# Optimization experiments

Measured on AMD Instinct MI355X. Metric: run time of the kernel, lower is better.

The kernel has to match this reference:

```python
import jax, jax.numpy as jnp
import numpy as np

N = 100_000
E = 1_600_000
IN_DIM = 21
HID = 256
OUT = 256


def setup_inputs() -> dict:
    key = jax.random.key(0)
    ks = jax.random.split(key, 10)
    node_scalar = jax.random.normal(ks[0], (N, IN_DIM), dtype=jnp.float32)
    edge_index = jax.random.randint(ks[1], (2, E), 0, N, dtype=jnp.int64)
    s_in = 1.0 / np.sqrt(IN_DIM)
    s_h = 1.0 / np.sqrt(HID)
    W_in = jax.random.uniform(ks[2], (IN_DIM, HID), jnp.float32, -s_in, s_in)
    b_in = jax.random.uniform(ks[3], (HID,), jnp.float32, -s_in, s_in)
    W_self = jax.random.uniform(ks[4], (HID, HID), jnp.float32, -s_h, s_h)
    b_self = jax.random.uniform(ks[5], (HID,), jnp.float32, -s_h, s_h)
    W_nei = jax.random.uniform(ks[6], (HID, HID), jnp.float32, -s_h, s_h)
    b_nei = jax.random.uniform(ks[7], (HID,), jnp.float32, -s_h, s_h)
    W_out = jax.random.uniform(ks[8], (HID, OUT), jnp.float32, -s_h, s_h)
    b_out = jax.random.uniform(ks[9], (OUT,), jnp.float32, -s_h, s_h)
    return {
        "node_scalar": node_scalar,
        "W_in": W_in, "b_in": b_in,
        "W_self": W_self, "b_self": b_self,
        "W_nei": W_nei, "b_nei": b_nei,
        "W_out": W_out, "b_out": b_out,
        "edge_index": edge_index,
    }


def reference(node_scalar, W_in, b_in, W_self, b_self, W_nei, b_nei, W_out, b_out, edge_index):
    # x = relu(Linear(node_scalar)); dropout is identity in eval mode
    x = jax.nn.relu(node_scalar @ W_in + b_in)           # (N, H)
    n = x.shape[0]
    src, dst = edge_index[0], edge_index[1]
    msg = x[src]                                          # (E, H) gather
    agg = jax.ops.segment_sum(msg, dst, num_segments=n)   # (N, H) scatter-add
    deg = jax.ops.segment_sum(jnp.ones((dst.shape[0],), dtype=x.dtype), dst, num_segments=n)
    agg = agg / jnp.maximum(deg, 1.0)[:, None]            # degree mean (clamp_min 1)
    h = jax.nn.relu(x @ W_self + b_self + agg @ W_nei + b_nei)
    g = h.mean(axis=0)                                    # global mean pool -> (H,)
    return g @ W_out + b_out                              # (OUT,)
```

## Files before the change

### kernel.cpp

```cpp
#include <hip/hip_runtime.h>
#include <hip/hip_bf16.h>

#define HID 256
#define IND 21
#define PB 6400
#define MAXB 512

typedef short short8 __attribute__((ext_vector_type(8)));
typedef float floatx16 __attribute__((ext_vector_type(16)));
typedef float floatx2 __attribute__((ext_vector_type(2)));

__device__ inline unsigned short f2bf(float f) {
  __hip_bfloat16 h = __float2bfloat16(f);
  union { __hip_bfloat16 h; unsigned short u; } c;
  c.h = h;
  return c.u;
}

__device__ inline unsigned int pk_bf16_trunc(floatx2 p) {
  union { float f; unsigned int u; } a, b;
  a.f = p.x; b.f = p.y;
  return (b.u & 0xffff0000u) | (a.u >> 16);
}

__device__ inline void acc8p(uint2 v, floatx2* a) {
  a[0] += __builtin_amdgcn_cvt_pk_f32_fp8((int)v.x, false);
  a[1] += __builtin_amdgcn_cvt_pk_f32_fp8((int)v.x, true);
  a[2] += __builtin_amdgcn_cvt_pk_f32_fp8((int)v.y, false);
  a[3] += __builtin_amdgcn_cvt_pk_f32_fp8((int)v.y, true);
}

__device__ inline short8 mk_s8(unsigned a, unsigned b, unsigned c, unsigned d) {
  union { uint4 u; short8 s; } x; x.u = make_uint4(a, b, c, d); return x.s;
}

__device__ inline short8 dec8(uint2 v) {
  unsigned w0 = pk_bf16_trunc(__builtin_amdgcn_cvt_pk_f32_fp8((int)v.x, false));
  unsigned w1 = pk_bf16_trunc(__builtin_amdgcn_cvt_pk_f32_fp8((int)v.x, true));
  unsigned w2 = pk_bf16_trunc(__builtin_amdgcn_cvt_pk_f32_fp8((int)v.y, false));
  unsigned w3 = pk_bf16_trunc(__builtin_amdgcn_cvt_pk_f32_fp8((int)v.y, true));
  return mk_s8(w0, w1, w2, w3);
}

__device__ inline void gl16(const unsigned char* g, unsigned char* l) {
  __builtin_amdgcn_global_load_lds(
      (const __attribute__((address_space(1))) unsigned char*)g,
      (__attribute__((address_space(3))) unsigned char*)l, 16, 0, 0);
}

__global__ __launch_bounds__(256) void k_front(
    const float* __restrict__ ns, const float* __restrict__ Win,
    const float* __restrict__ bin, uint2* __restrict__ xq2,
    uint2* __restrict__ Aqx,
    const float* __restrict__ Wself, const float* __restrict__ Wnei,
    unsigned short* __restrict__ Bf16,
    const int* __restrict__ dst, int* __restrict__ bcnt,
    int N, int E, int nb2, int G1) {
  int blk = blockIdx.x;
  int tid = threadIdx.x;
  if (blk < G1) {
    __shared__ float s[8][IND];
    __shared__ float fx[8][257];
    int nb = blk * 8;
    if (tid < 8 * IND) {
      int idx = nb * IND + tid;
      s[tid / IND][tid % IND] = (idx < N * IND) ? ns[idx] : 0.f;
    }
    float w[IND];
#pragma unroll
    for (int k = 0; k < IND; k++) w[k] = Win[k * HID + tid];
    float b = bin[tid];
    __syncthreads();
#pragma unroll
    for (int j = 0; j < 8; j++) {
      float acc = b;
#pragma unroll
      for (int k = 0; k < IND; k++) acc += s[j][k] * w[k];
      fx[j][tid] = acc > 0.f ? acc : 0.f;
    }
    __syncthreads();
    {
      int j = tid & 7, u = tid >> 3;
      int node = nb + j;
      if (node < N) {
        const float* fp = &fx[j][u * 8];
        int lo0 = __builtin_amdgcn_cvt_pk_fp8_f32(fp[0], fp[1], 0, false);
        int w0  = __builtin_amdgcn_cvt_pk_fp8_f32(fp[2], fp[3], lo0, true);
        int lo1 = __builtin_amdgcn_cvt_pk_fp8_f32(fp[4], fp[5], 0, false);
        int w1  = __builtin_amdgcn_cvt_pk_fp8_f32(fp[6], fp[7], lo1, true);
        uint2 val = make_uint2((unsigned)w0, (unsigned)w1);
        xq2[(size_t)node * 32 + u] = val;
        int g = node >> 5, row = node & 31, c = u >> 1, hi = u & 1;
        Aqx[(size_t)(g * 16 + c) * 64 + hi * 32 + row] = val;
      }
    }
  } else if (blk < G1 + 256) {
    int n = blk - G1;
    int ct = n >> 5, l5 = n & 31;
#pragma unroll
    for (int t = 0; t < 2; t++) {
      int k = tid + t * 256;
      float v = (k < HID) ? Wself[k * HID + n] : Wnei[(k - HID) * HID + n];
      int c = k >> 4, kin = k & 15;
      int lane = (kin >> 3) * 32 + l5;
      int j = kin & 7;
      Bf16[(size_t)((c * 8 + ct) * 64 + lane) * 8 + j] = f2bf(v);
    }
  } else {
    __shared__ int lh[MAXB];
    int e0 = (blk - G1 - 256) * PB;
    for (int b = tid; b < nb2; b += 256) lh[b] = 0;
    __syncthreads();
    int c = min(PB, E - e0);
    for (int i = tid; i < c; i += 256) atomicAdd(&lh[dst[e0 + i] >> 8], 1);
    __syncthreads();
    for (int b = tid; b < nb2; b += 256)
      if (lh[b]) atomicAdd(&bcnt[b], lh[b]);
  }
}

__global__ __launch_bounds__(512) void k_bscan(
    const int* __restrict__ bcnt, int* __restrict__ bbase, int* __restrict__ bcur,
    int* __restrict__ row_start, int E, int N, int nb2) {
  __shared__ int ts[512];
  int tid = threadIdx.x;
  int v = (tid < nb2) ? bcnt[tid] : 0;
  ts[tid] = v;
  __syncthreads();
  for (int off = 1; off < 512; off <<= 1) {
    int t = (tid >= off) ? ts[tid - off] : 0;
    __syncthreads();
    ts[tid] += t;
    __syncthreads();
  }
  if (tid < nb2) { bbase[tid] = ts[tid] - v; bcur[tid] = ts[tid] - v; }
  if (tid == 0) { bbase[nb2] = E; row_start[N] = E; }
}

__global__ __launch_bounds__(256) void k_part(
    const int* __restrict__ src, const int* __restrict__ dst,
    int* __restrict__ bcur, unsigned int* __restrict__ ebuf, int E, int nb2) {
  __shared__ int lh[MAXB];
  int tid = threadIdx.x;
  int e0 = blockIdx.x * PB;
  for (int b = tid; b < nb2; b += 256) lh[b] = 0;
  __syncthreads();
  int cnt = min(PB, E - e0);
  for (int i = tid; i < cnt; i += 256) atomicAdd(&lh[dst[e0 + i] >> 8], 1);
  __syncthreads();
  for (int b = tid; b < nb2; b += 256) {
    int c = lh[b];
    lh[b] = (c > 0) ? atomicAdd(&bcur[b], c) : 0;
  }
  __syncthreads();
  for (int i = tid; i < cnt; i += 256) {
    int s = src[e0 + i];
    int d = dst[e0 + i];
    int pos = atomicAdd(&lh[d >> 8], 1);
    ebuf[pos] = ((unsigned)s << 8) | ((unsigned)d & 255u);
  }
}

__global__ __launch_bounds__(256) void k_fill2(
    const unsigned int* __restrict__ ebuf, const int* __restrict__ bbase,
    int* __restrict__ row_start, unsigned int* __restrict__ csr, int N) {
  __shared__ int lcnt[256];
  __shared__ int lcur[256];
  __shared__ int ts[256];
  int b = blockIdx.x;
  int tid = threadIdx.x;
  int start = bbase[b], end = bbase[b + 1];
  lcnt[tid] = 0;
  __syncthreads();
  for (int i = start + tid; i < end; i += 256)
    atomicAdd(&lcnt[ebuf[i] & 255u], 1);
  __syncthreads();
  int v = lcnt[tid];
  ts[tid] = v;
  __syncthreads();
  for (int off = 1; off < 256; off <<= 1) {
    int t = (tid >= off) ? ts[tid - off] : 0;
    __syncthreads();
    ts[tid] += t;
    __syncthreads();
  }
  int excl = start + ts[tid] - v;
  int node = (b << 8) + tid;
  if (node < N) row_start[node] = excl;
  lcur[tid] = excl;
  __syncthreads();
  for (int i = start + tid; i < end; i += 256) {
    unsigned int e = ebuf[i];
    int pos = atomicAdd(&lcur[e & 255u], 1);
    csr[pos] = e & ~255u;
  }
}

__global__ __launch_bounds__(256) void k_agg(
    const unsigned char* __restrict__ xqb, const unsigned int* __restrict__ csrb,
    const int* __restrict__ row_start, uint2* __restrict__ Aqagg, int N) {
  __shared__ uint2 ld[8][33];
  int tid = threadIdx.x;
  int lane = tid & 63;
  int w = tid >> 6;
  int half = lane >> 5;
  int l32 = lane & 31;
  unsigned lo = (unsigned)(l32 * 8);

  int nl = w * 2 + half;
  int wid = blockIdx.x * 8 + nl;
  int cw = (wid < N) ? wid : (N - 1);
  int start = row_start[cw];
  int end = row_start[cw + 1];
  int c = end - start;
  floatx2 a[4], b[4], d[4], e[4];
#pragma unroll
  for (int j = 0; j < 4; j++) {
    a[j] = (floatx2){0.f, 0.f}; b[j] = (floatx2){0.f, 0.f};
    d[j] = (floatx2){0.f, 0.f}; e[j] = (floatx2){0.f, 0.f};
  }
  int i = 0;
  while (i < c) {
    int nb = min(32, c - i);
    int sel = (l32 < nb) ? l32 : 0;
    unsigned idx = csrb[start + i + sel];
    int j = 0;
    for (; j + 8 <= nb; j += 8) {
      unsigned o0 = (unsigned)__shfl((int)idx, j + 0, 32) + lo;
      unsigned o1 = (unsigned)__shfl((int)idx, j + 1, 32) + lo;
      unsigned o2 = (unsigned)__shfl((int)idx, j + 2, 32) + lo;
      unsigned o3 = (unsigned)__shfl((int)idx, j + 3, 32) + lo;
      unsigned o4 = (unsigned)__shfl((int)idx, j + 4, 32) + lo;
      unsigned o5 = (unsigned)__shfl((int)idx, j + 5, 32) + lo;
      unsigned o6 = (unsigned)__shfl((int)idx, j + 6, 32) + lo;
      unsigned o7 = (unsigned)__shfl((int)idx, j + 7, 32) + lo;
      uint2 v0 = *(const uint2*)(xqb + o0);
      uint2 v1 = *(const uint2*)(xqb + o1);
      uint2 v2 = *(const uint2*)(xqb + o2);
      uint2 v3 = *(const uint2*)(xqb + o3);
      uint2 v4 = *(const uint2*)(xqb + o4);
      uint2 v5 = *(const uint2*)(xqb + o5);
      uint2 v6 = *(const uint2*)(xqb + o6);
      uint2 v7 = *(const uint2*)(xqb + o7);
      acc8p(v0, a); acc8p(v1, b); acc8p(v2, d); acc8p(v3, e);
      acc8p(v4, a); acc8p(v5, b); acc8p(v6, d); acc8p(v7, e);
    }
    for (; j + 4 <= nb; j += 4) {
      unsigned o0 = (unsigned)__shfl((int)idx, j + 0, 32) + lo;
      unsigned o1 = (unsigned)__shfl((int)idx, j + 1, 32) + lo;
      unsigned o2 = (unsigned)__shfl((int)idx, j + 2, 32) + lo;
      unsigned o3 = (unsigned)__shfl((int)idx, j + 3, 32) + lo;
      uint2 v0 = *(const uint2*)(xqb + o0);
      uint2 v1 = *(const uint2*)(xqb + o1);
      uint2 v2 = *(const uint2*)(xqb + o2);
      uint2 v3 = *(const uint2*)(xqb + o3);
      acc8p(v0, a); acc8p(v1, b); acc8p(v2, d); acc8p(v3, e);
    }
    for (; j < nb; j++) {
      unsigned o0 = (unsigned)__shfl((int)idx, j, 32) + lo;
      uint2 v0 = *(const uint2*)(xqb + o0);
      acc8p(v0, a);
    }
    i += nb;
  }
#pragma unroll
  for (int j = 0; j < 4; j++) a[j] += b[j] + d[j] + e[j];

  float inv = 1.0f / fmaxf((float)c, 1.0f);
  float f[8];
#pragma unroll
  for (int j = 0; j < 4; j++) {
    f[2 * j] = a[j].x * inv;
    f[2 * j + 1] = a[j].y * inv;
  }
  int lo0 = __builtin_amdgcn_cvt_pk_fp8_f32(f[0], f[1], 0, false);
  int w0  = __builtin_amdgcn_cvt_pk_fp8_f32(f[2], f[3], lo0, true);
  int lo1 = __builtin_amdgcn_cvt_pk_fp8_f32(f[4], f[5], 0, false);
  int w1  = __builtin_amdgcn_cvt_pk_fp8_f32(f[6], f[7], lo1, true);
  ld[nl][l32] = make_uint2((unsigned)w0, (unsigned)w1);
  __syncthreads();

  int g = blockIdx.x >> 2;
  int r0 = (blockIdx.x & 3) * 8;
  int s = tid >> 3, j = tid & 7;
  Aqagg[(size_t)g * 1024 + (size_t)s * 32 + r0 + j] = ld[j][s];
}

__global__ __launch_bounds__(256, 3) void k_h(
    const unsigned char* __restrict__ Aqx, const unsigned char* __restrict__ Aqagg,
    const unsigned char* __restrict__ Bf8, const float* __restrict__ bself,
    const float* __restrict__ bnei, float* __restrict__ gsum, int N, int nfull) {
  __shared__ __align__(16) unsigned char As[2][8192];
  __shared__ __align__(16) unsigned char Bs[2][16384];
  __shared__ float colsum[128];
  int bid = blockIdx.x;
  int bx, by;
  if (bid < nfull) {
    bx = (bid >> 4) * 8 + (bid & 7);
    by = (bid >> 3) & 1;
  } else {
    int rem = bid - nfull;
    bx = (nfull >> 1) + (rem >> 1);
    by = rem & 1;
  }
  int tid = threadIdx.x;
  int lane = tid & 63;
  int w = tid >> 6;
  int wr = w >> 1, wc = w & 1;
  int l32 = lane & 31, half = lane >> 5;
  int rowBase = bx * 128;

  if (tid < 128) colsum[tid] = 0.f;

  floatx16 acc[2][2];
#pragma unroll
  for (int i = 0; i < 2; i++)
#pragma unroll
    for (int j = 0; j < 2; j++) acc[i][j] = (floatx16)(0.f);

  size_t a_grp = (size_t)(bx * 4 + w) * 16 * 512;
  int lb = lane * 16;

  {
    const unsigned char* asrc = Aqx + a_grp + lb;
    gl16(asrc, As[0] + w * 2048);
    gl16(asrc + 1024, As[0] + w * 2048 + 1024);
#pragma unroll
    for (int fi = 0; fi < 4; fi++) {
      int ctg = by * 4 + fi;
      gl16(Bf8 + (size_t)(w * 8 + ctg) * 1024 + lb, Bs[0] + (w * 4 + fi) * 1024);
    }
  }

  for (int ch = 0; ch < 8; ch++) {
    int buf = ch & 1;
    __syncthreads();
    if (ch < 7) {
      int cn = ch + 1;
      const unsigned char* Aq = (cn < 4) ? Aqx : Aqagg;
      const unsigned char* asrc = Aq + a_grp + (size_t)(cn & 3) * 2048 + lb;
      unsigned char* ad = As[buf ^ 1] + w * 2048;
      gl16(asrc, ad);
      gl16(asrc + 1024, ad + 1024);
#pragma unroll
      for (int fi = 0; fi < 4; fi++) {
        int cg = cn * 4 + w;
        int ctg = by * 4 + fi;
        gl16(Bf8 + (size_t)(cg * 8 + ctg) * 1024 + lb,
             Bs[buf ^ 1] + (w * 4 + fi) * 1024);
      }
    }
#pragma unroll
    for (int cl = 0; cl < 4; cl++) {
      short8 afr[2];
#pragma unroll
      for (int rt = 0; rt < 2; rt++) {
        uint2 av = *(const uint2*)&As[buf][(wr * 2 + rt) * 2048 + cl * 512 + lane * 8];
        afr[rt] = dec8(av);
      }
#pragma unroll
      for (int ctw = 0; ctw < 2; ctw++) {
        short8 bfr = *(const short8*)&Bs[buf][(cl * 4 + wc * 2 + ctw) * 1024 + lane * 16];
#pragma unroll
        for (int rt = 0; rt < 2; rt++)
          acc[rt][ctw] = __builtin_amdgcn_mfma_f32_32x32x16_bf16(
              afr[rt], bfr, acc[rt][ctw], 0, 0, 0);
      }
    }
  }

#pragma unroll
  for (int ctw = 0; ctw < 2; ctw++) {
    int lcol = (wc * 2 + ctw) * 32 + l32;
    int gcol = by * 128 + lcol;
    float bb = bself[gcol] + bnei[gcol];
    float psum = 0.f;
#pragma unroll
    for (int rt = 0; rt < 2; rt++) {
#pragma unroll
      for (int r = 0; r < 16; r++) {
        int rw = rowBase + wr * 64 + rt * 32 + (r & 3) + 8 * (r >> 2) + 4 * half;
        float v = acc[rt][ctw][r] + bb;
        v = v > 0.f ? v : 0.f;
        if (rw < N) psum += v;
      }
    }
    atomicAdd(&colsum[lcol], psum);
  }
  __syncthreads();
  if (tid < 128) atomicAdd(&gsum[by * 128 + tid], colsum[tid]);
}

__global__ __launch_bounds__(HID) void k_out(
    const float* __restrict__ gsum, const float* __restrict__ Wout,
    const float* __restrict__ bout, float* __restrict__ out, float invN) {
  __shared__ float g[HID];
  int c = threadIdx.x;
  g[c] = gsum[c] * invN;
  __syncthreads();
  float acc = bout[c];
#pragma unroll 8
  for (int k = 0; k < HID; k++) acc += g[k] * Wout[k * HID + c];
  out[c] = acc;
}

extern "C" void kernel_launch(void* const* d_in, const int* in_sizes, int n_in,
                              void* d_out, int out_size, void* d_ws, size_t ws_size,
                              hipStream_t stream) {
  const float* ns    = (const float*)d_in[0];
  const float* Win   = (const float*)d_in[1];
  const float* bin   = (const float*)d_in[2];
  const float* Wself = (const float*)d_in[3];
  const float* bself = (const float*)d_in[4];
  const float* Wnei  = (const float*)d_in[5];
  const float* bnei  = (const float*)d_in[6];
  const float* Wout  = (const float*)d_in[7];
  const float* bout  = (const float*)d_in[8];
  const int*   eidx  = (const int*)d_in[9];

  int N = in_sizes[0] / IND;
  int E = in_sizes[9] / 2;
  const int* src = eidx;
  const int* dst = eidx + E;
  int nb2 = (N + 255) >> 8;
  int nbx = (N + 127) / 128;
  size_t NGU = (size_t)nbx * 4 * 16 * 64;

  unsigned int* xq     = (unsigned int*)d_ws;
  uint2* Aqx           = (uint2*)(xq + (size_t)N * 64);
  uint2* Aqagg         = Aqx + NGU;
  unsigned short* Bf16 = (unsigned short*)(Aqagg + NGU);
  unsigned int* csr  = (unsigned int*)(Bf16 + 256 * 512);
  unsigned int* ebuf = csr + E;
  int* row_start = (int*)(ebuf + E);
  int* bcnt      = row_start + N + 1;
  float* gsum    = (float*)(bcnt + MAXB);
  int* bbase     = (int*)(gsum + HID);
  int* bcur      = bbase + MAXB + 1;

  hipMemsetAsync(bcnt, 0, (MAXB + HID) * sizeof(int), stream);

  int G1 = (N + 7) / 8;
  int pgrid = (E + PB - 1) / PB;
  k_front<<<G1 + 256 + pgrid, 256, 0, stream>>>(
      ns, Win, bin, (uint2*)xq, Aqx, Wself, Wnei, Bf16, dst, bcnt,
      N, E, nb2, G1);

  k_bscan<<<1, 512, 0, stream>>>(bcnt, bbase, bcur, row_start, E, N, nb2);
  k_part<<<pgrid, 256, 0, stream>>>(src, dst, bcur, ebuf, E, nb2);
  k_fill2<<<nb2, 256, 0, stream>>>(ebuf, bbase, row_start, csr, N);

  int agrid = (N + 7) / 8;
  k_agg<<<agrid, 256, 0, stream>>>((const unsigned char*)xq, csr, row_start,
                                   Aqagg, N);

  int nblocks = nbx * 2;
  int nfull = (nblocks / 16) * 16;
  k_h<<<nblocks, 256, 0, stream>>>((const unsigned char*)Aqx,
                                   (const unsigned char*)Aqagg,
                                   (const unsigned char*)Bf16,
                                   bself, bnei, gsum, N, nfull);

  k_out<<<1, HID, 0, stream>>>(gsum, Wout, bout, (float*)d_out, 1.0f / (float)N);
}
```

Before: 285.1 us.

## Load full A tile to LDS upfront and stream B fragments through registers

The k_h GEMM kernel now copies the block's entire fp8 A tile (64KB) into LDS in one go and drops the per-chunk double-buffered LDS staging and the barrier inside the loop. B fragments are read directly from global memory into registers, with the next chunk prefetched. Occupancy hint drops from 3 to 2 blocks per CU because of the larger LDS footprint. Separately, the front kernel's 21-wide input dot product reads LDS as float4 vectors instead of scalars.

Measured after the change: 278.5 us. 2.3% less time.

```diff
diff --git a/kernel.cpp b/kernel.cpp
--- a/kernel.cpp
+++ b/kernel.cpp
@@ -59,7 +59,7 @@
   int blk = blockIdx.x;
   int tid = threadIdx.x;
   if (blk < G1) {
-    __shared__ float s[8][IND];
+    __shared__ __align__(16) float s[8][24];
     __shared__ float fx[8][257];
     int nb = blk * 8;
     if (tid < 8 * IND) {
@@ -74,8 +74,14 @@
 #pragma unroll
     for (int j = 0; j < 8; j++) {
       float acc = b;
-#pragma unroll
-      for (int k = 0; k < IND; k++) acc += s[j][k] * w[k];
+      const float4* sp = (const float4*)&s[j][0];
+#pragma unroll
+      for (int k4 = 0; k4 < 5; k4++) {
+        float4 t = sp[k4];
+        acc += t.x * w[k4 * 4] + t.y * w[k4 * 4 + 1] +
+               t.z * w[k4 * 4 + 2] + t.w * w[k4 * 4 + 3];
+      }
+      acc += s[j][20] * w[20];
       fx[j][tid] = acc > 0.f ? acc : 0.f;
     }
     __syncthreads();
@@ -286,12 +292,11 @@
   Aqagg[(size_t)g * 1024 + (size_t)s * 32 + r0 + j] = ld[j][s];
 }
 
-__global__ __launch_bounds__(256, 3) void k_h(
+__global__ __launch_bounds__(256, 2) void k_h(
     const unsigned char* __restrict__ Aqx, const unsigned char* __restrict__ Aqagg,
     const unsigned char* __restrict__ Bf8, const float* __restrict__ bself,
     const float* __restrict__ bnei, float* __restrict__ gsum, int N, int nfull) {
-  __shared__ __align__(16) unsigned char As[2][8192];
-  __shared__ __align__(16) unsigned char Bs[2][16384];
+  __shared__ __align__(16) unsigned char As[65536];
   __shared__ float colsum[128];
   int bid = blockIdx.x;
   int bx, by;
@@ -318,54 +323,53 @@
 #pragma unroll
     for (int j = 0; j < 2; j++) acc[i][j] = (floatx16)(0.f);
 
-  size_t a_grp = (size_t)(bx * 4 + w) * 16 * 512;
+  size_t a_grp = (size_t)(bx * 4 + w) * 8192;
   int lb = lane * 16;
-
-  {
-    const unsigned char* asrc = Aqx + a_grp + lb;
-    gl16(asrc, As[0] + w * 2048);
-    gl16(asrc + 1024, As[0] + w * 2048 + 1024);
-#pragma unroll
-    for (int fi = 0; fi < 4; fi++) {
-      int ctg = by * 4 + fi;
-      gl16(Bf8 + (size_t)(w * 8 + ctg) * 1024 + lb, Bs[0] + (w * 4 + fi) * 1024);
-    }
-  }
-
+#pragma unroll
   for (int ch = 0; ch < 8; ch++) {
-    int buf = ch & 1;
-    __syncthreads();
+    const unsigned char* Aq = (ch < 4) ? Aqx : Aqagg;
+    const unsigned char* srcp = Aq + a_grp + (size_t)(ch & 3) * 2048 + lb;
+    unsigned char* dstp = As + (size_t)(w * 8 + ch) * 2048;
+    gl16(srcp, dstp);
+    gl16(srcp + 1024, dstp + 1024);
+  }
+
+  size_t bgrp = ((size_t)(by * 4 + wc * 2) * 64 + lane) * 16;
+  short8 b0[4], b1[4];
+#pragma unroll
+  for (int cl = 0; cl < 4; cl++) {
+    const unsigned char* bb = Bf8 + bgrp + (size_t)cl * 8192;
+    b0[cl] = *(const short8*)bb;
+    b1[cl] = *(const short8*)(bb + 1024);
+  }
+
+  __syncthreads();
+
+  for (int ch = 0; ch < 8; ch++) {
+    short8 n0[4], n1[4];
     if (ch < 7) {
-      int cn = ch + 1;
-      const unsigned char* Aq = (cn < 4) ? Aqx : Aqagg;
-      const unsigned char* asrc = Aq + a_grp + (size_t)(cn & 3) * 2048 + lb;
-      unsigned char* ad = As[buf ^ 1] + w * 2048;
-      gl16(asrc, ad);
-      gl16(asrc + 1024, ad + 1024);
-#pragma unroll
-      for (int fi = 0; fi < 4; fi++) {
-        int cg = cn * 4 + w;
-        int ctg = by * 4 + fi;
-        gl16(Bf8 + (size_t)(cg * 8 + ctg) * 1024 + lb,
-             Bs[buf ^ 1] + (w * 4 + fi) * 1024);
+#pragma unroll
+      for (int cl = 0; cl < 4; cl++) {
+        const unsigned char* bb =
+            Bf8 + bgrp + ((size_t)(ch + 1) * 4 + cl) * 8192;
+        n0[cl] = *(const short8*)bb;
+        n1[cl] = *(const short8*)(bb + 1024);
       }
     }
 #pragma unroll
     for (int cl = 0; cl < 4; cl++) {
-      short8 afr[2];
-#pragma unroll
-      for (int rt = 0; rt < 2; rt++) {
-        uint2 av = *(const uint2*)&As[buf][(wr * 2 + rt) * 2048 + cl * 512 + lane * 8];
-        afr[rt] = dec8(av);
-      }
-#pragma unroll
-      for (int ctw = 0; ctw < 2; ctw++) {
-        short8 bfr = *(const short8*)&Bs[buf][(cl * 4 + wc * 2 + ctw) * 1024 + lane * 16];
-#pragma unroll
-        for (int rt = 0; rt < 2; rt++)
-          acc[rt][ctw] = __builtin_amdgcn_mfma_f32_32x32x16_bf16(
-              afr[rt], bfr, acc[rt][ctw], 0, 0, 0);
-      }
+      short8 afr0 = dec8(*(const uint2*)&As[
+          ((size_t)(wr * 2 + 0) * 8 + ch) * 2048 + cl * 512 + lane * 8]);
+      short8 afr1 = dec8(*(const uint2*)&As[
+          ((size_t)(wr * 2 + 1) * 8 + ch) * 2048 + cl * 512 + lane * 8]);
+      acc[0][0] = __builtin_amdgcn_mfma_f32_32x32x16_bf16(afr0, b0[cl], acc[0][0], 0, 0, 0);
+      acc[1][0] = __builtin_amdgcn_mfma_f32_32x32x16_bf16(afr1, b0[cl], acc[1][0], 0, 0, 0);
+      acc[0][1] = __builtin_amdgcn_mfma_f32_32x32x16_bf16(afr0, b1[cl], acc[0][1], 0, 0, 0);
+      acc[1][1] = __builtin_amdgcn_mfma_f32_32x32x16_bf16(afr1, b1[cl], acc[1][1], 0, 0, 0);
+    }
+    if (ch < 7) {
+#pragma unroll
+      for (int cl = 0; cl < 4; cl++) { b0[cl] = n0[cl]; b1[cl] = n1[cl]; }
     }
   }
 
```
